# Kernel optimization log

Measured on AMD Instinct MI355X. Metric: run time of the kernel, lower is better.

## Reference

```python
import math
import jax, jax.numpy as jnp
import numpy as np

B, H, W, DIM = 4, 128, 128, 256
NUM_HEADS = 8
BLOCK = 8
HALO = 3
WIN = BLOCK + 2 * HALO            # 14
DH_QK = DIM // NUM_HEADS          # 32 (make_divisible(256*1.0)//8)
DH_V = DIM // NUM_HEADS           # 32
SCALE = DH_QK ** (-0.5)


def abs_pos_embed(win, halo, dim, temperature=10000.0, scale=2 * math.pi, eps=1e-6):
    # dim is half the channel dim; output has 2*dim channels
    ones = jnp.ones((win, win), jnp.float32)
    y_embed = jnp.cumsum(ones, 0)
    x_embed = jnp.cumsum(ones, 1)
    y_embed = y_embed / (y_embed[-1:, :] + eps) * scale
    x_embed = x_embed / (x_embed[:, -1:] + eps) * scale
    dim_t = temperature ** (2 * (jnp.arange(dim) // 2).astype(jnp.float32) / dim)

    def enc(e):
        p = e[:, :, None] / dim_t
        # interleave sin of even channels, cos of odd channels
        return jnp.stack([jnp.sin(p[:, :, 0::2]), jnp.cos(p[:, :, 1::2])], axis=3).reshape(win, win, -1)

    pos = jnp.concatenate([enc(y_embed), enc(x_embed)], axis=2)
    q_pos = pos[halo:-halo, halo:-halo].reshape(-1, 2 * dim)     # [block^2, 2*dim]
    k_pos = pos.reshape(-1, 2 * dim)
    return q_pos, k_pos


def extract_windows(x_pad, nh, nw, block, win):
    ih = (jnp.arange(nh) * block)[:, None] + jnp.arange(win)[None, :]
    iw = (jnp.arange(nw) * block)[:, None] + jnp.arange(win)[None, :]
    return x_pad[:, ih[:, None, :, None], iw[None, :, None, :], :]


def setup_inputs() -> dict:
    key = jax.random.key(0)
    ks = jax.random.split(key, 6)
    return {
        "x": jax.random.normal(ks[0], (B, H, W, DIM), jnp.float32),
        "Wq": jax.random.normal(ks[1], (DIM, NUM_HEADS * DH_QK), jnp.float32) * 0.05,
        "Wk": jax.random.normal(ks[2], (DIM, NUM_HEADS * DH_QK), jnp.float32) * 0.05,
        "Wv": jax.random.normal(ks[3], (DIM, NUM_HEADS * DH_V), jnp.float32) * 0.05,
        "Wproj": jax.random.normal(ks[4], (NUM_HEADS * DH_V, NUM_HEADS * DH_V), jnp.float32) * 0.05,
        "bproj": jnp.zeros((NUM_HEADS * DH_V,), jnp.float32),
    }


def reference(x, Wq, Wk, Wv, Wproj, bproj):
    Bx, Hx, Wx, C = x.shape
    nh, nw = Hx // BLOCK, Wx // BLOCK
    nb = nh * nw
    q_win = BLOCK * BLOCK
    kv_win = WIN * WIN

    q_pos, k_pos = abs_pos_embed(WIN, HALO, C // 2)

    # query blocks: [B, nb, block^2, C]
    qb = x.reshape(Bx, nh, BLOCK, nw, BLOCK, C).transpose(0, 1, 3, 2, 4, 5).reshape(Bx, nb, q_win, C)
    q = (qb + q_pos[None, None]) @ Wq                                   # [B,nb,q_win,Cqk]
    q = q.reshape(Bx, nb, q_win, NUM_HEADS, DH_QK).transpose(0, 3, 1, 2, 4)

    x_pad = jnp.pad(x, ((0, 0), (HALO, HALO), (HALO, HALO), (0, 0)))
    kv = extract_windows(x_pad, nh, nw, BLOCK, WIN).reshape(Bx, nb, kv_win, C)
    k = (kv + k_pos[None, None]) @ Wk
    v = kv @ Wv
    k = k.reshape(Bx, nb, kv_win, NUM_HEADS, DH_QK).transpose(0, 3, 1, 2, 4)
    v = v.reshape(Bx, nb, kv_win, NUM_HEADS, DH_V).transpose(0, 3, 1, 2, 4)

    attn = jnp.einsum('bhnqd,bhnkd->bhnqk', q * SCALE, k)              # [B,h,nb,q_win,kv_win]

    # halo padding validity mask
    valid = extract_windows(
        jnp.pad(jnp.ones((1, Hx, Wx, 1), attn.dtype), ((0, 0), (HALO, HALO), (HALO, HALO), (0, 0))),
        nh, nw, BLOCK, WIN,
    ).reshape(1, nb, kv_win)
    invalid = valid[:, None, :, None, :] == 0                          # [1,1,nb,1,kv_win]
    neg = -jnp.finfo(attn.dtype).max
    attn = jnp.where(invalid, neg, attn)
    attn = jax.nn.softmax(attn, axis=-1)

    out = jnp.einsum('bhnqk,bhnkd->bhnqd', attn, v)                    # [B,h,nb,q_win,dhv]
    out = out.reshape(Bx, NUM_HEADS, nh, nw, BLOCK, BLOCK, DH_V)
    out = out.transpose(0, 2, 4, 3, 5, 1, 6).reshape(Bx, Hx, Wx, NUM_HEADS * DH_V)
    return out @ Wproj + bproj
```

## Files before the change

kernel.cpp:

```cpp
#include <hip/hip_runtime.h>


using bf16x8 = __attribute__((ext_vector_type(8))) short;
using f32x4  = __attribute__((ext_vector_type(4))) float;

__device__ __forceinline__ float bf2f(unsigned short u) {
  return __uint_as_float(((unsigned int)u) << 16);
}
__device__ __forceinline__ unsigned short f2bf(float f) {
  unsigned int x = __float_as_uint(f);
  x += 0x7fffu + ((x >> 16) & 1u);
  return (unsigned short)(x >> 16);
}
__device__ __forceinline__ unsigned int pack2(float a, float b) {
  return (unsigned int)f2bf(a) | ((unsigned int)f2bf(b) << 16);
}
__device__ __forceinline__ int div14(int p) { return (p * 4682) >> 16; }

__global__ __launch_bounds__(256) void pos_proj_kernel(
    const float* __restrict__ Wq, const float* __restrict__ Wk,
    float* __restrict__ PK, float* __restrict__ PQ) {
  __shared__ float pr[256];
  const int row = blockIdx.x, o = threadIdx.x;
  const float* Wm;
  float* dst;
  int ii, jj;
  if (row < 208) {
    if (row >= 196) { PK[row * 256 + o] = 0.f; return; }
    ii = row / 14; jj = row % 14;
    Wm = Wk; dst = PK + row * 256;
  } else {
    int qp = row - 208;
    ii = (qp >> 3) + 3; jj = (qp & 7) + 3;
    Wm = Wq; dst = PQ + qp * 256;
  }
  const int cl = o & 127, mfreq = cl >> 1;
  float t = powf(10000.f, (float)mfreq * (1.f / 64.f));
  float base = (o < 128) ? (float)(ii + 1) : (float)(jj + 1);
  float arg = base * (6.283185307179586f / 14.000001f) / t;
  pr[o] = (cl & 1) ? cosf(arg) : sinf(arg);
  __syncthreads();
  float acc = 0.f;
  for (int c = 0; c < 256; ++c) acc = fmaf(pr[c], Wm[c * 256 + o], acc);
  dst[o] = acc;
}

__global__ __launch_bounds__(256) void wtrans2_kernel(
    const float* __restrict__ Wq, const float* __restrict__ Wk,
    const float* __restrict__ Wv, const float* __restrict__ Wp,
    unsigned short* __restrict__ Wt) {
  __shared__ unsigned short sW[256 * 40];
  const int mat = blockIdx.x >> 3, kc = blockIdx.x & 7;
  const float* src = (mat == 0) ? Wq : (mat == 1) ? Wk : (mat == 2) ? Wv : Wp;
  const int tid = threadIdx.x;
  for (int t = tid; t < 2048; t += 256) {
    int k = t >> 6, sg = t & 63;
    float4 v = *(const float4*)&src[(kc * 32 + k) * 256 + sg * 4];
    sW[(sg * 4 + 0) * 40 + k] = f2bf(v.x);
    sW[(sg * 4 + 1) * 40 + k] = f2bf(v.y);
    sW[(sg * 4 + 2) * 40 + k] = f2bf(v.z);
    sW[(sg * 4 + 3) * 40 + k] = f2bf(v.w);
  }
  __syncthreads();
  unsigned short* dst = Wt + mat * 65536 + kc * 8192;
  for (int t = tid; t < 1024; t += 256) {
    int n = t >> 2, sg = t & 3;
    *(uint4*)&dst[n * 32 + sg * 8] = *(const uint4*)&sW[n * 40 + sg * 8];
  }
}

struct QkvLds {
  union {
    struct {
      unsigned short sA[128 * 40];
      unsigned short sB[128 * 40];
    } s;
    unsigned short sT[64 * 136];
  } u;
  float sPQ[8 * 128];
};

__global__ __launch_bounds__(256, 3) void qkv_gemm_kernel(
    const float* __restrict__ xg, const unsigned short* __restrict__ Wt,
    const float* __restrict__ PQ,
    unsigned short* __restrict__ XQ, unsigned short* __restrict__ XK,
    unsigned short* __restrict__ XVt) {
  __shared__ QkvLds sm;
  const int mat = blockIdx.x;
  const int tb = blockIdx.y;
  const int m0 = (tb >> 1) << 7;
  const int n0 = (tb & 1) << 7;
  const int tid = threadIdx.x;
  const int wave = tid >> 6, lane = tid & 63, q = lane >> 4, r = lane & 15;
  const unsigned short* Wb = Wt + mat * 65536 + n0 * 32;

  if (mat == 0) {
    const int y7 = (m0 >> 7) & 7;
    const int rr = tid >> 5, cc = tid & 31;
    *(float4*)&sm.sPQ[rr * 128 + cc * 4] =
        *(const float4*)&PQ[(y7 * 8 + rr) * 256 + n0 + cc * 4];
  }

  const int rowA = tid >> 2, segA = tid & 3;
  const float* aptr = xg + ((m0 + rowA) << 8) + segA * 8;
  const int rowB = tid >> 1, segB = (tid & 1) << 4;
  const unsigned short* bptr = Wb + tid * 16;

  f32x4 acc[2][8];
#pragma unroll
  for (int mt = 0; mt < 2; ++mt)
#pragma unroll
    for (int nt = 0; nt < 8; ++nt) acc[mt][nt] = (f32x4){0.f, 0.f, 0.f, 0.f};

  float4 a00 = *(const float4*)(aptr);
  float4 a01 = *(const float4*)(aptr + 4);
  float4 a10 = *(const float4*)(aptr + 16384);
  float4 a11 = *(const float4*)(aptr + 16384 + 4);
  uint4 b0 = *(const uint4*)(bptr);
  uint4 b1 = *(const uint4*)(bptr + 8);

  for (int kc = 0; kc < 8; ++kc) {
    if (kc) __syncthreads();
    {
      uint4 w;
      w.x = pack2(a00.x, a00.y); w.y = pack2(a00.z, a00.w);
      w.z = pack2(a01.x, a01.y); w.w = pack2(a01.z, a01.w);
      *(uint4*)&sm.u.s.sA[rowA * 40 + segA * 8] = w;
      w.x = pack2(a10.x, a10.y); w.y = pack2(a10.z, a10.w);
      w.z = pack2(a11.x, a11.y); w.w = pack2(a11.z, a11.w);
      *(uint4*)&sm.u.s.sA[(rowA + 64) * 40 + segA * 8] = w;
      *(uint4*)&sm.u.s.sB[rowB * 40 + segB] = b0;
      *(uint4*)&sm.u.s.sB[rowB * 40 + segB + 8] = b1;
    }
    __syncthreads();
    if (kc < 7) {
      const float* ap = aptr + (kc + 1) * 32;
      a00 = *(const float4*)(ap);
      a01 = *(const float4*)(ap + 4);
      a10 = *(const float4*)(ap + 16384);
      a11 = *(const float4*)(ap + 16384 + 4);
      const unsigned short* bp = bptr + (kc + 1) * 8192;
      b0 = *(const uint4*)(bp);
      b1 = *(const uint4*)(bp + 8);
    }
    bf16x8 a0 = *(const bf16x8*)&sm.u.s.sA[(wave * 32 + r) * 40 + q * 8];
    bf16x8 a1 = *(const bf16x8*)&sm.u.s.sA[(wave * 32 + 16 + r) * 40 + q * 8];
#pragma unroll
    for (int nt = 0; nt < 8; ++nt) {
      bf16x8 bw = *(const bf16x8*)&sm.u.s.sB[(nt * 16 + r) * 40 + q * 8];
      acc[0][nt] = __builtin_amdgcn_mfma_f32_16x16x32_bf16(a0, bw, acc[0][nt], 0, 0, 0);
      acc[1][nt] = __builtin_amdgcn_mfma_f32_16x16x32_bf16(a1, bw, acc[1][nt], 0, 0, 0);
    }
  }

  if (mat == 2) {
    __syncthreads();
#pragma unroll
    for (int c4 = 0; c4 < 2; ++c4) {
      if (c4) __syncthreads();
#pragma unroll
      for (int mt = 0; mt < 2; ++mt)
#pragma unroll
        for (int n4 = 0; n4 < 4; ++n4)
#pragma unroll
          for (int g = 0; g < 4; ++g) {
            int ch = n4 * 16 + r;
            int pr = wave * 32 + mt * 16 + q * 4 + g;
            sm.u.sT[ch * 136 + pr] = f2bf(acc[mt][c4 * 4 + n4][g]);
          }
      __syncthreads();
      for (int t = tid; t < 1024; t += 256) {
        int ch = t >> 4, sg = t & 15;
        *(uint4*)&XVt[((n0 + c4 * 64 + ch) << 16) + m0 + sg * 8] =
            *(const uint4*)&sm.u.sT[ch * 136 + sg * 8];
      }
    }
  } else {
    unsigned short* dst = (mat == 0) ? XQ : XK;
#pragma unroll
    for (int mt = 0; mt < 2; ++mt)
#pragma unroll
      for (int nt = 0; nt < 8; ++nt)
#pragma unroll
        for (int g = 0; g < 4; ++g) {
          int lrow = wave * 32 + mt * 16 + q * 4 + g;
          float v = acc[mt][nt][g];
          if (mat == 0) v += sm.sPQ[(lrow & 7) * 128 + nt * 16 + r];
          dst[((m0 + lrow) << 8) + n0 + nt * 16 + r] = f2bf(v);
        }
  }
}

struct alignas(16) SMH {
  unsigned short sK[196 * 40];
  unsigned short sVt[32 * 232];
  unsigned short sU[64 * 40];
};

__global__ __launch_bounds__(256, 4) void halo_kernel(
    const unsigned short* XQ,
    const unsigned short* __restrict__ XK,
    const unsigned short* __restrict__ XVt,
    const float* __restrict__ PK,
    unsigned short* XO) {
  __shared__ SMH sm;
  const int wid = blockIdx.x;
  const int h = wid & 7, win = wid >> 3;
  const int b = win >> 8, widx = win & 255;
  const int wy = widx >> 4, wx = widx & 15;
  const int hc = h * 32;
  const int tid = threadIdx.x;
  const int wave = tid >> 6, lane = tid & 63, q = lane >> 4, r = lane & 15;
  const bool interior = (unsigned)(wy - 1) < 14u && (unsigned)(wx - 1) < 14u;
  const int ybase = wy * 8 - 3, xbase = wx * 8 - 3;
  constexpr float SCALE = 0.17677669529663687f;

  for (int idx = tid; idx < 1152; idx += 256) {
    int rr = idx / 36, c2 = idx - rr * 36;
    sm.sVt[rr * 232 + 196 + c2] = 0;
  }

  if (interior) {
    for (int t = tid; t < 784; t += 256) {
      int p = t >> 2, seg = t & 3;
      int i = div14(p), j = p - i * 14;
      int pix = (b * 128 + ybase + i) * 128 + xbase + j;
      bf16x8 kv = *(const bf16x8*)&XK[(pix << 8) + hc + seg * 8];
      const float4* pk4 = (const float4*)(PK + (p << 8) + hc + seg * 8);
      float4 f0 = pk4[0], f1 = pk4[1];
      uint4 w;
      w.x = pack2(bf2f((unsigned short)kv[0]) + f0.x, bf2f((unsigned short)kv[1]) + f0.y);
      w.y = pack2(bf2f((unsigned short)kv[2]) + f0.z, bf2f((unsigned short)kv[3]) + f0.w);
      w.z = pack2(bf2f((unsigned short)kv[4]) + f1.x, bf2f((unsigned short)kv[5]) + f1.y);
      w.w = pack2(bf2f((unsigned short)kv[6]) + f1.z, bf2f((unsigned short)kv[7]) + f1.w);
      *(uint4*)&sm.sK[p * 40 + seg * 8] = w;
    }
    for (int t = tid; t < 448; t += 256) {
      int c = div14(t), i = t - c * 14;
      int pix0 = (b * 128 + ybase + i) * 128 + xbase;
      const unsigned int* src = (const unsigned int*)(XVt + ((hc + c) << 16) + pix0 - 1);
      unsigned int d[8];
#pragma unroll
      for (int k = 0; k < 8; ++k) d[k] = src[k];
      int base = c * 232 + i * 14;
#pragma unroll
      for (int k = 0; k < 7; ++k)
        *(unsigned int*)&sm.sVt[base + k * 2] = (d[k] >> 16) | (d[k + 1] << 16);
    }
  } else {
    for (int t = tid; t < 784; t += 256) {
      int p = t >> 2, seg = t & 3;
      int i = div14(p), j = p - i * 14;
      int y = ybase + i, x = xbase + j;
      uint4 w = {0u, 0u, 0u, 0u};
      if ((unsigned)y < 128u && (unsigned)x < 128u) {
        int pix = (b * 128 + y) * 128 + x;
        bf16x8 kv = *(const bf16x8*)&XK[(pix << 8) + hc + seg * 8];
        const float4* pk4 = (const float4*)(PK + (p << 8) + hc + seg * 8);
        float4 f0 = pk4[0], f1 = pk4[1];
        w.x = pack2(bf2f((unsigned short)kv[0]) + f0.x, bf2f((unsigned short)kv[1]) + f0.y);
        w.y = pack2(bf2f((unsigned short)kv[2]) + f0.z, bf2f((unsigned short)kv[3]) + f0.w);
        w.z = pack2(bf2f((unsigned short)kv[4]) + f1.x, bf2f((unsigned short)kv[5]) + f1.y);
        w.w = pack2(bf2f((unsigned short)kv[6]) + f1.z, bf2f((unsigned short)kv[7]) + f1.w);
      }
      *(uint4*)&sm.sK[p * 40 + seg * 8] = w;
    }
    for (int t = tid; t < 448; t += 256) {
      int c = div14(t), i = t - c * 14;
      int y = ybase + i;
      unsigned int o[7] = {0u, 0u, 0u, 0u, 0u, 0u, 0u};
      if ((unsigned)y < 128u) {
        const unsigned short* row = XVt + ((hc + c) << 16) + (b * 128 + y) * 128;
#pragma unroll
        for (int k = 0; k < 7; ++k) {
          int x0 = xbase + 2 * k, x1 = x0 + 1;
          unsigned int lo = ((unsigned)x0 < 128u) ? row[x0] : 0u;
          unsigned int hi = ((unsigned)x1 < 128u) ? row[x1] : 0u;
          o[k] = lo | (hi << 16);
        }
      }
      int base = c * 232 + i * 14;
#pragma unroll
      for (int k = 0; k < 7; ++k) *(unsigned int*)&sm.sVt[base + k * 2] = o[k];
    }
  }
  {
    int m = tid >> 2, seg = tid & 3;
    int pix = (b * 128 + wy * 8 + (m >> 3)) * 128 + wx * 8 + (m & 7);
    *(uint4*)&sm.sU[m * 40 + seg * 8] = *(const uint4*)&XQ[(pix << 8) + hc + seg * 8];
  }
  __syncthreads();

  bf16x8 aq = *(const bf16x8*)&sm.sU[(wave * 16 + r) * 40 + q * 8];
  f32x4 s[14];
#pragma unroll
  for (int nt = 0; nt < 14; ++nt) {
    bf16x8 bk = *(const bf16x8*)&sm.sK[(nt * 16 + r) * 40 + q * 8];
    f32x4 z = {0.f, 0.f, 0.f, 0.f};
    s[nt] = __builtin_amdgcn_mfma_f32_16x16x32_bf16(aq, bk, z, 0, 0, 0);
  }
  if (interior) {
#pragma unroll
    for (int nt = 0; nt < 12; ++nt)
#pragma unroll
      for (int g = 0; g < 4; ++g) s[nt][g] *= SCALE;
#pragma unroll
    for (int g = 0; g < 4; ++g) {
      s[12][g] = (r < 4) ? s[12][g] * SCALE : -1e30f;
      s[13][g] = -1e30f;
    }
  } else {
#pragma unroll
    for (int nt = 0; nt < 14; ++nt) {
      int n = nt * 16 + r;
      int i = div14(n), j = n - i * 14;
      int y = ybase + i, x = xbase + j;
      bool valid = (n < 196) && ((unsigned)y < 128u) && ((unsigned)x < 128u);
#pragma unroll
      for (int g = 0; g < 4; ++g) s[nt][g] = valid ? s[nt][g] * SCALE : -1e30f;
    }
  }
  float mx[4] = {-1e30f, -1e30f, -1e30f, -1e30f};
#pragma unroll
  for (int nt = 0; nt < 14; ++nt)
#pragma unroll
    for (int g = 0; g < 4; ++g) mx[g] = fmaxf(mx[g], s[nt][g]);
#pragma unroll
  for (int d = 1; d < 16; d <<= 1)
#pragma unroll
    for (int g = 0; g < 4; ++g) mx[g] = fmaxf(mx[g], __shfl_xor(mx[g], d));
  float sum[4] = {0.f, 0.f, 0.f, 0.f};
#pragma unroll
  for (int nt = 0; nt < 14; ++nt)
#pragma unroll
    for (int g = 0; g < 4; ++g) {
      float e = __expf(s[nt][g] - mx[g]);
      s[nt][g] = e; sum[g] += e;
    }
#pragma unroll
  for (int d = 1; d < 16; d <<= 1)
#pragma unroll
    for (int g = 0; g < 4; ++g) sum[g] += __shfl_xor(sum[g], d);
  float inv[4];
#pragma unroll
  for (int g = 0; g < 4; ++g) inv[g] = 1.f / sum[g];
#pragma unroll
  for (int nt = 0; nt < 14; ++nt)
#pragma unroll
    for (int g = 0; g < 4; ++g) s[nt][g] *= inv[g];

  f32x4 ov[2];
  ov[0] = (f32x4){0.f, 0.f, 0.f, 0.f}; ov[1] = ov[0];
#pragma unroll
  for (int ck = 0; ck < 7; ++ck) {
#pragma unroll
    for (int tq = 0; tq < 2; ++tq)
#pragma unroll
      for (int g = 0; g < 4; ++g)
        sm.sU[(wave * 16 + q * 4 + g) * 40 + tq * 16 + r] = f2bf(s[ck * 2 + tq][g]);
    bf16x8 ap = *(const bf16x8*)&sm.sU[(wave * 16 + r) * 40 + q * 8];
#pragma unroll
    for (int t2 = 0; t2 < 2; ++t2) {
      bf16x8 bv = *(const bf16x8*)&sm.sVt[(t2 * 16 + r) * 232 + ck * 32 + q * 8];
      ov[t2] = __builtin_amdgcn_mfma_f32_16x16x32_bf16(ap, bv, ov[t2], 0, 0, 0);
    }
  }
#pragma unroll
  for (int t2 = 0; t2 < 2; ++t2)
#pragma unroll
    for (int g = 0; g < 4; ++g)
      sm.sU[(wave * 16 + q * 4 + g) * 40 + t2 * 16 + r] = f2bf(ov[t2][g]);
  {
    int m = tid >> 2, seg = tid & 3;
    int pix = (b * 128 + wy * 8 + (m >> 3)) * 128 + wx * 8 + (m & 7);
    bf16x8 o8 = *(const bf16x8*)&sm.sU[m * 40 + seg * 8];
    *(uint4*)&XO[(pix << 8) + hc + seg * 8] = *(uint4*)&o8;
  }
}

__global__ __launch_bounds__(256, 3) void out_proj_kernel(
    const unsigned short* __restrict__ XO, const unsigned short* __restrict__ Wt,
    const float* __restrict__ bp, float* __restrict__ out) {
  __shared__ unsigned short sA[128 * 40];
  __shared__ unsigned short sB[128 * 40];
  const int tb = blockIdx.x;
  const int m0 = (tb >> 1) << 7, n0 = (tb & 1) << 7;
  const int tid = threadIdx.x;
  const int wave = tid >> 6, lane = tid & 63, q = lane >> 4, r = lane & 15;
  const unsigned short* Wb = Wt + 3 * 65536 + n0 * 32;

  const int rowA = tid >> 2, segA = tid & 3;
  const unsigned short* aptr = XO + ((m0 + rowA) << 8) + segA * 8;
  const int rowB = tid >> 1, segB = (tid & 1) << 4;
  const unsigned short* bptr = Wb + tid * 16;

  f32x4 acc[2][8];
#pragma unroll
  for (int nt = 0; nt < 8; ++nt) {
    float bv = bp[n0 + nt * 16 + r];
    acc[0][nt] = (f32x4){bv, bv, bv, bv};
    acc[1][nt] = (f32x4){bv, bv, bv, bv};
  }

  uint4 pa0 = *(const uint4*)(aptr);
  uint4 pa1 = *(const uint4*)(aptr + 16384);
  uint4 b0 = *(const uint4*)(bptr);
  uint4 b1 = *(const uint4*)(bptr + 8);

  for (int kc = 0; kc < 8; ++kc) {
    if (kc) __syncthreads();
    *(uint4*)&sA[rowA * 40 + segA * 8] = pa0;
    *(uint4*)&sA[(rowA + 64) * 40 + segA * 8] = pa1;
    *(uint4*)&sB[rowB * 40 + segB] = b0;
    *(uint4*)&sB[rowB * 40 + segB + 8] = b1;
    __syncthreads();
    if (kc < 7) {
      const unsigned short* ap = aptr + (kc + 1) * 32;
      pa0 = *(const uint4*)(ap);
      pa1 = *(const uint4*)(ap + 16384);
      const unsigned short* bpc = bptr + (kc + 1) * 8192;
      b0 = *(const uint4*)(bpc);
      b1 = *(const uint4*)(bpc + 8);
    }
    bf16x8 a0 = *(const bf16x8*)&sA[(wave * 32 + r) * 40 + q * 8];
    bf16x8 a1 = *(const bf16x8*)&sA[(wave * 32 + 16 + r) * 40 + q * 8];
#pragma unroll
    for (int nt = 0; nt < 8; ++nt) {
      bf16x8 bw = *(const bf16x8*)&sB[(nt * 16 + r) * 40 + q * 8];
      acc[0][nt] = __builtin_amdgcn_mfma_f32_16x16x32_bf16(a0, bw, acc[0][nt], 0, 0, 0);
      acc[1][nt] = __builtin_amdgcn_mfma_f32_16x16x32_bf16(a1, bw, acc[1][nt], 0, 0, 0);
    }
  }
#pragma unroll
  for (int mt = 0; mt < 2; ++mt)
#pragma unroll
    for (int nt = 0; nt < 8; ++nt)
#pragma unroll
      for (int g = 0; g < 4; ++g) {
        int row = m0 + wave * 32 + mt * 16 + q * 4 + g;
        out[(row << 8) + n0 + nt * 16 + r] = acc[mt][nt][g];
      }
}

extern "C" void kernel_launch(void* const* d_in, const int* in_sizes, int n_in,
                              void* d_out, int out_size, void* d_ws, size_t ws_size,
                              hipStream_t stream) {
  (void)in_sizes; (void)n_in; (void)out_size;
  const float* xg = (const float*)d_in[0];
  const float* Wq = (const float*)d_in[1];
  const float* Wk = (const float*)d_in[2];
  const float* Wv = (const float*)d_in[3];
  const float* Wp = (const float*)d_in[4];
  const float* bp = (const float*)d_in[5];
  float* out = (float*)d_out;

  if (ws_size < 101466112u) return;

  char* ws = (char*)d_ws;
  unsigned short* XQO = (unsigned short*)(ws);
  unsigned short* XK  = (unsigned short*)(ws + 33554432u);
  unsigned short* XVt = (unsigned short*)(ws + 67108864u);
  unsigned short* Wt  = (unsigned short*)(ws + 100663296u);
  float* PK = (float*)(ws + 101187584u);
  float* PQ = (float*)(ws + 101400576u);

  pos_proj_kernel<<<dim3(272), dim3(256), 0, stream>>>(Wq, Wk, PK, PQ);
  wtrans2_kernel<<<dim3(32), dim3(256), 0, stream>>>(Wq, Wk, Wv, Wp, Wt);
  qkv_gemm_kernel<<<dim3(3, 1024), dim3(256), 0, stream>>>(xg, Wt, PQ, XQO, XK, XVt);
  halo_kernel<<<dim3(8192), dim3(256), 0, stream>>>(XQO, XK, XVt, PK, XQO);
  out_proj_kernel<<<dim3(1024), dim3(256), 0, stream>>>(XQO, Wt, bp, out);
}
```

Measured before the change: 315.2 us.

## Double-buffer LDS tiles in QKV and output projection GEMMs

Converts the QKV and output-projection GEMM main loops to use two LDS buffers with two register staging sets. The next k-chunk is packed and written to the alternate buffer while the current one is being consumed, which halves the barriers per k-step and overlaps global loads with MFMA work. It also packs the V-transpose epilogue stores into 64-bit LDS writes. The cost is doubled LDS per block and more live registers, which may reduce occupancy.

```diff
diff --git a/kernel.cpp b/kernel.cpp
--- a/kernel.cpp
+++ b/kernel.cpp
@@ -72,8 +72,8 @@
 struct QkvLds {
   union {
     struct {
-      unsigned short sA[128 * 40];
-      unsigned short sB[128 * 40];
+      unsigned short sA[2][128 * 40];
+      unsigned short sB[2][128 * 40];
     } s;
     unsigned short sT[64 * 136];
   } u;
@@ -112,62 +112,82 @@
 #pragma unroll
     for (int nt = 0; nt < 8; ++nt) acc[mt][nt] = (f32x4){0.f, 0.f, 0.f, 0.f};
 
-  float4 a00 = *(const float4*)(aptr);
-  float4 a01 = *(const float4*)(aptr + 4);
-  float4 a10 = *(const float4*)(aptr + 16384);
-  float4 a11 = *(const float4*)(aptr + 16384 + 4);
-  uint4 b0 = *(const uint4*)(bptr);
-  uint4 b1 = *(const uint4*)(bptr + 8);
-
-  for (int kc = 0; kc < 8; ++kc) {
-    if (kc) __syncthreads();
-    {
-      uint4 w;
-      w.x = pack2(a00.x, a00.y); w.y = pack2(a00.z, a00.w);
-      w.z = pack2(a01.x, a01.y); w.w = pack2(a01.z, a01.w);
-      *(uint4*)&sm.u.s.sA[rowA * 40 + segA * 8] = w;
-      w.x = pack2(a10.x, a10.y); w.y = pack2(a10.z, a10.w);
-      w.z = pack2(a11.x, a11.y); w.w = pack2(a11.z, a11.w);
-      *(uint4*)&sm.u.s.sA[(rowA + 64) * 40 + segA * 8] = w;
-      *(uint4*)&sm.u.s.sB[rowB * 40 + segB] = b0;
-      *(uint4*)&sm.u.s.sB[rowB * 40 + segB + 8] = b1;
-    }
+  float4 xa00, xa01, xa10, xa11; uint4 xb0, xb1;
+  float4 ya00, ya01, ya10, ya11; uint4 yb0, yb1;
+
+#define QKV_LOAD(S, KC)                                          \
+  {                                                              \
+    const float* ap_ = aptr + (KC) * 32;                         \
+    S##a00 = *(const float4*)(ap_);                              \
+    S##a01 = *(const float4*)(ap_ + 4);                          \
+    S##a10 = *(const float4*)(ap_ + 16384);                      \
+    S##a11 = *(const float4*)(ap_ + 16384 + 4);                  \
+    const unsigned short* bp_ = bptr + (KC) * 8192;              \
+    S##b0 = *(const uint4*)(bp_);                                \
+    S##b1 = *(const uint4*)(bp_ + 8);                            \
+  }
+
+#define QKV_PACKWRITE(BUF, S)                                    \
+  {                                                              \
+    uint4 w_;                                                    \
+    w_.x = pack2(S##a00.x, S##a00.y); w_.y = pack2(S##a00.z, S##a00.w); \
+    w_.z = pack2(S##a01.x, S##a01.y); w_.w = pack2(S##a01.z, S##a01.w); \
+    *(uint4*)&sm.u.s.sA[BUF][rowA * 40 + segA * 8] = w_;         \
+    w_.x = pack2(S##a10.x, S##a10.y); w_.y = pack2(S##a10.z, S##a10.w); \
+    w_.z = pack2(S##a11.x, S##a11.y); w_.w = pack2(S##a11.z, S##a11.w); \
+    *(uint4*)&sm.u.s.sA[BUF][(rowA + 64) * 40 + segA * 8] = w_;  \
+    *(uint4*)&sm.u.s.sB[BUF][rowB * 40 + segB] = S##b0;          \
+    *(uint4*)&sm.u.s.sB[BUF][rowB * 40 + segB + 8] = S##b1;      \
+  }
+
+#define QKV_COMPUTE(BUF)                                                         \
+  {                                                                              \
+    bf16x8 a0_ = *(const bf16x8*)&sm.u.s.sA[BUF][(wave * 32 + r) * 40 + q * 8];  \
+    bf16x8 a1_ = *(const bf16x8*)&sm.u.s.sA[BUF][(wave * 32 + 16 + r) * 40 + q * 8]; \
+    _Pragma("unroll")                                                            \
+    for (int nt = 0; nt < 8; ++nt) {                                             \
+      bf16x8 bw_ = *(const bf16x8*)&sm.u.s.sB[BUF][(nt * 16 + r) * 40 + q * 8];  \
+      acc[0][nt] = __builtin_amdgcn_mfma_f32_16x16x32_bf16(a0_, bw_, acc[0][nt], 0, 0, 0); \
+      acc[1][nt] = __builtin_amdgcn_mfma_f32_16x16x32_bf16(a1_, bw_, acc[1][nt], 0, 0, 0); \
+    }                                                                            \
+  }
+
+  QKV_LOAD(x, 0)
+  QKV_PACKWRITE(0, x)
+  QKV_LOAD(y, 1)
+  __syncthreads();
+
+#pragma unroll
+  for (int k2 = 0; k2 < 4; ++k2) {
+    const int kc = 2 * k2;
+    QKV_COMPUTE(0)
+    QKV_PACKWRITE(1, y)
+    if (kc < 6) QKV_LOAD(x, kc + 2)
     __syncthreads();
-    if (kc < 7) {
-      const float* ap = aptr + (kc + 1) * 32;
-      a00 = *(const float4*)(ap);
-      a01 = *(const float4*)(ap + 4);
-      a10 = *(const float4*)(ap + 16384);
-      a11 = *(const float4*)(ap + 16384 + 4);
-      const unsigned short* bp = bptr + (kc + 1) * 8192;
-      b0 = *(const uint4*)(bp);
-      b1 = *(const uint4*)(bp + 8);
-    }
-    bf16x8 a0 = *(const bf16x8*)&sm.u.s.sA[(wave * 32 + r) * 40 + q * 8];
-    bf16x8 a1 = *(const bf16x8*)&sm.u.s.sA[(wave * 32 + 16 + r) * 40 + q * 8];
-#pragma unroll
-    for (int nt = 0; nt < 8; ++nt) {
-      bf16x8 bw = *(const bf16x8*)&sm.u.s.sB[(nt * 16 + r) * 40 + q * 8];
-      acc[0][nt] = __builtin_amdgcn_mfma_f32_16x16x32_bf16(a0, bw, acc[0][nt], 0, 0, 0);
-      acc[1][nt] = __builtin_amdgcn_mfma_f32_16x16x32_bf16(a1, bw, acc[1][nt], 0, 0, 0);
-    }
-  }
+    QKV_COMPUTE(1)
+    if (kc < 6) QKV_PACKWRITE(0, x)
+    if (kc < 5) QKV_LOAD(y, kc + 3)
+    __syncthreads();
+  }
+#undef QKV_LOAD
+#undef QKV_PACKWRITE
+#undef QKV_COMPUTE
 
   if (mat == 2) {
-    __syncthreads();
 #pragma unroll
     for (int c4 = 0; c4 < 2; ++c4) {
       if (c4) __syncthreads();
 #pragma unroll
       for (int mt = 0; mt < 2; ++mt)
 #pragma unroll
-        for (int n4 = 0; n4 < 4; ++n4)
-#pragma unroll
-          for (int g = 0; g < 4; ++g) {
-            int ch = n4 * 16 + r;
-            int pr = wave * 32 + mt * 16 + q * 4 + g;
-            sm.u.sT[ch * 136 + pr] = f2bf(acc[mt][c4 * 4 + n4][g]);
-          }
+        for (int n4 = 0; n4 < 4; ++n4) {
+          int ch = n4 * 16 + r;
+          int prb = wave * 32 + mt * 16 + q * 4;
+          uint2 w;
+          w.x = pack2(acc[mt][c4 * 4 + n4][0], acc[mt][c4 * 4 + n4][1]);
+          w.y = pack2(acc[mt][c4 * 4 + n4][2], acc[mt][c4 * 4 + n4][3]);
+          *(uint2*)&sm.u.sT[ch * 136 + prb] = w;
+        }
       __syncthreads();
       for (int t = tid; t < 1024; t += 256) {
         int ch = t >> 4, sg = t & 15;
@@ -381,8 +401,8 @@
 __global__ __launch_bounds__(256, 3) void out_proj_kernel(
     const unsigned short* __restrict__ XO, const unsigned short* __restrict__ Wt,
     const float* __restrict__ bp, float* __restrict__ out) {
-  __shared__ unsigned short sA[128 * 40];
-  __shared__ unsigned short sB[128 * 40];
+  __shared__ unsigned short sA[2][128 * 40];
+  __shared__ unsigned short sB[2][128 * 40];
   const int tb = blockIdx.x;
   const int m0 = (tb >> 1) << 7, n0 = (tb & 1) << 7;
   const int tid = threadIdx.x;
@@ -402,35 +422,60 @@
     acc[1][nt] = (f32x4){bv, bv, bv, bv};
   }
 
-  uint4 pa0 = *(const uint4*)(aptr);
-  uint4 pa1 = *(const uint4*)(aptr + 16384);
-  uint4 b0 = *(const uint4*)(bptr);
-  uint4 b1 = *(const uint4*)(bptr + 8);
-
-  for (int kc = 0; kc < 8; ++kc) {
-    if (kc) __syncthreads();
-    *(uint4*)&sA[rowA * 40 + segA * 8] = pa0;
-    *(uint4*)&sA[(rowA + 64) * 40 + segA * 8] = pa1;
-    *(uint4*)&sB[rowB * 40 + segB] = b0;
-    *(uint4*)&sB[rowB * 40 + segB + 8] = b1;
+  uint4 xa0, xa1, xb0, xb1;
+  uint4 ya0, ya1, yb0, yb1;
+
+#define OP_LOAD(S, KC)                                      \
+  {                                                         \
+    const unsigned short* ap_ = aptr + (KC) * 32;           \
+    S##a0 = *(const uint4*)(ap_);                           \
+    S##a1 = *(const uint4*)(ap_ + 16384);                   \
+    const unsigned short* bp_ = bptr + (KC) * 8192;         \
+    S##b0 = *(const uint4*)(bp_);                           \
+    S##b1 = *(const uint4*)(bp_ + 8);                       \
+  }
+
+#define OP_WRITE(BUF, S)                                    \
+  {                                                         \
+    *(uint4*)&sA[BUF][rowA * 40 + segA * 8] = S##a0;        \
+    *(uint4*)&sA[BUF][(rowA + 64) * 40 + segA * 8] = S##a1; \
+    *(uint4*)&sB[BUF][rowB * 40 + segB] = S##b0;            \
+    *(uint4*)&sB[BUF][rowB * 40 + segB + 8] = S##b1;        \
+  }
+
+#define OP_COMPUTE(BUF)                                                        \
+  {                                                                            \
+    bf16x8 a0_ = *(const bf16x8*)&sA[BUF][(wave * 32 + r) * 40 + q * 8];       \
+    bf16x8 a1_ = *(const bf16x8*)&sA[BUF][(wave * 32 + 16 + r) * 40 + q * 8];  \
+    _Pragma("unroll")                                                          \
+    for (int nt = 0; nt < 8; ++nt) {                                           \
+      bf16x8 bw_ = *(const bf16x8*)&sB[BUF][(nt * 16 + r) * 40 + q * 8];       \
+      acc[0][nt] = __builtin_amdgcn_mfma_f32_16x16x32_bf16(a0_, bw_, acc[0][nt], 0, 0, 0); \
+      acc[1][nt] = __builtin_amdgcn_mfma_f32_16x16x32_bf16(a1_, bw_, acc[1][nt], 0, 0, 0); \
+    }                                                                          \
+  }
+
+  OP_LOAD(x, 0)
+  OP_WRITE(0, x)
+  OP_LOAD(y, 1)
+  __syncthreads();
+
+#pragma unroll
+  for (int k2 = 0; k2 < 4; ++k2) {
+    const int kc = 2 * k2;
+    OP_COMPUTE(0)
+    OP_WRITE(1, y)
+    if (kc < 6) OP_LOAD(x, kc + 2)
     __syncthreads();
-    if (kc < 7) {
-      const unsigned short* ap = aptr + (kc + 1) * 32;
-      pa0 = *(const uint4*)(ap);
-      pa1 = *(const uint4*)(ap + 16384);
-      const unsigned short* bpc = bptr + (kc + 1) * 8192;
-      b0 = *(const uint4*)(bpc);
-      b1 = *(const uint4*)(bpc + 8);
-    }
-    bf16x8 a0 = *(const bf16x8*)&sA[(wave * 32 + r) * 40 + q * 8];
-    bf16x8 a1 = *(const bf16x8*)&sA[(wave * 32 + 16 + r) * 40 + q * 8];
-#pragma unroll
-    for (int nt = 0; nt < 8; ++nt) {
-      bf16x8 bw = *(const bf16x8*)&sB[(nt * 16 + r) * 40 + q * 8];
-      acc[0][nt] = __builtin_amdgcn_mfma_f32_16x16x32_bf16(a0, bw, acc[0][nt], 0, 0, 0);
-      acc[1][nt] = __builtin_amdgcn_mfma_f32_16x16x32_bf16(a1, bw, acc[1][nt], 0, 0, 0);
-    }
-  }
+    OP_COMPUTE(1)
+    if (kc < 6) OP_WRITE(0, x)
+    if (kc < 5) OP_LOAD(y, kc + 3)
+    __syncthreads();
+  }
+#undef OP_LOAD
+#undef OP_WRITE
+#undef OP_COMPUTE
+
 #pragma unroll
   for (int mt = 0; mt < 2; ++mt)
 #pragma unroll
```

After: 357.9 us. 13.6% more time.
